# Kernel optimization log

Measured on AMD Instinct MI355X. Metric: run time of the kernel, lower is better.

The kernel has to match this reference:

```python
import jax, jax.numpy as jnp
import numpy as np

EPS = 1e-5
GROUPS = 8


def conv2d(x, w, b, pad):
    y = jax.lax.conv_general_dilated(
        x, w, window_strides=(1, 1), padding=[(pad, pad), (pad, pad)],
        dimension_numbers=('NCHW', 'OIHW', 'NCHW'))
    return y + b[None, :, None, None]


def setup_inputs() -> dict:
    key = jax.random.key(0)
    ks = jax.random.split(key, 8)
    b, c, h, w = 32, 256, 56, 56
    cg = c // GROUPS
    x = jax.random.normal(ks[0], (b, c, h, w), dtype=jnp.float32)
    w1 = jax.random.normal(ks[1], (cg, cg, 1, 1), dtype=jnp.float32) * 0.05
    b1 = jnp.zeros((cg,), dtype=jnp.float32)
    w3a = jax.random.normal(ks[2], (cg, cg, 3, 3), dtype=jnp.float32) * 0.05
    b3a = jnp.zeros((cg,), dtype=jnp.float32)
    w3b = jax.random.normal(ks[3], (c, c, 3, 3), dtype=jnp.float32) * 0.02
    b3b = jnp.zeros((c,), dtype=jnp.float32)
    gn_w = jnp.ones((cg,), dtype=jnp.float32)
    gn_b = jnp.zeros((cg,), dtype=jnp.float32)
    return {"x": x, "w1": w1, "b1": b1, "w3a": w3a, "b3a": b3a,
            "w3b": w3b, "b3b": b3b, "gn_w": gn_w, "gn_b": gn_b}


def reference(x, w1, b1, w3a, b3a, w3b, b3b, gn_w, gn_b):
    b, c, h, w = x.shape
    cg = c // GROUPS
    bg = b * GROUPS
    gx = x.reshape(bg, cg, h, w)

    # spatial attention on grouped channels
    x_h = gx.mean(axis=3, keepdims=True)                       # [bg,cg,h,1]
    x_w = gx.mean(axis=2, keepdims=True).transpose(0, 1, 3, 2)  # [bg,cg,w,1]
    hw = conv2d(jnp.concatenate([x_h, x_w], axis=2), w1, b1, 0)
    xh, xw = hw[:, :, :h], hw[:, :, h:]
    x0 = gx * jax.nn.sigmoid(xh) * jax.nn.sigmoid(xw.transpose(0, 1, 3, 2))

    # GroupNorm with num_groups == num_channels (per-channel over HxW)
    mu = x0.mean(axis=(2, 3), keepdims=True)
    var = x0.var(axis=(2, 3), keepdims=True)
    x1 = (x0 - mu) / jnp.sqrt(var + EPS) * gn_w[None, :, None, None] + gn_b[None, :, None, None]

    x2 = conv2d(gx, w3a, b3a, 1)

    # channel softmax-matmul attention (per group)
    x11 = jax.nn.softmax(x1.mean(axis=(2, 3)), axis=-1)[:, None, :]  # [bg,1,cg]
    x12 = x1.reshape(bg, cg, h * w)
    x21 = jax.nn.softmax(x2.mean(axis=(2, 3)), axis=-1)[:, None, :]
    x22 = x2.reshape(bg, cg, h * w)
    weights1 = (jnp.matmul(x11, x22) + jnp.matmul(x21, x12)).reshape(bg, 1, h, w)

    # BatchNorm2d(affine=False), batch statistics (training mode)
    xr = x0.reshape(b, c, h, w)
    bm = xr.mean(axis=(0, 2, 3), keepdims=True)
    bv = xr.var(axis=(0, 2, 3), keepdims=True)
    x3 = (xr - bm) / jnp.sqrt(bv + EPS)

    x4 = conv2d(x, w3b, b3b, 1)

    # spatial softmax-matmul attention over full channels
    x31 = jax.nn.softmax(x3.mean(axis=1).reshape(b, 1, h * w), axis=-1)  # [b,1,hw]
    x32 = x3.reshape(b, c, h * w).transpose(0, 2, 1)                     # [b,hw,c]
    x41 = jax.nn.softmax(x4.mean(axis=1).reshape(b, 1, h * w), axis=-1)
    x42 = x4.reshape(b, c, h * w).transpose(0, 2, 1)
    weights2 = (jnp.matmul(x31, x42) + jnp.matmul(x41, x32)).reshape(b, c, 1, 1)

    return (gx * jax.nn.sigmoid(weights1)).reshape(b, c, h, w) + x * jax.nn.sigmoid(weights2)
```

## Files before the change

### kernel.cpp

```cpp
#include <hip/hip_runtime.h>
#include <math.h>

#define B  32
#define C  256
#define HH 56
#define WW 56
#define HW 3136
#define G  8
#define CG 32
#define BG 256
#define GC 8192
#define EPSF 1e-5f

typedef __attribute__((ext_vector_type(8))) short short8;
typedef __attribute__((ext_vector_type(4))) float f32x4;

#define GLOAD16(g, l) __builtin_amdgcn_global_load_lds( \
    (const __attribute__((address_space(1))) void*)(g), \
    (__attribute__((address_space(3))) void*)(l), 16, 0, 0)

__device__ __forceinline__ float sigmoidf_(float v){ return 1.0f/(1.0f+__expf(-v)); }
__device__ __forceinline__ unsigned short f2bf(float v){
  unsigned u = __builtin_bit_cast(unsigned, v);
  u = u + 0x7FFFu + ((u>>16)&1u);
  return (unsigned short)(u>>16);
}

__global__ void k1_rowcol(const float* __restrict__ x, float* __restrict__ rowm, float* __restrict__ colm){
  int gc = blockIdx.x;
  __shared__ float t[56][57];
  const float* xp = x + (size_t)gc*HW;
  for(int idx=threadIdx.x; idx<HW; idx+=blockDim.x) t[idx/56][idx%56] = xp[idx];
  __syncthreads();
  int tid = threadIdx.x;
  if(tid < 56){
    float s=0.f;
    #pragma unroll 8
    for(int j=0;j<56;j++) s+=t[tid][j];
    rowm[gc*56+tid] = s*(1.0f/56.0f);
  } else if(tid>=64 && tid<120){
    int j=tid-64; float s=0.f;
    #pragma unroll 8
    for(int i=0;i<56;i++) s+=t[i][j];
    colm[gc*56+j] = s*(1.0f/56.0f);
  }
}

__global__ void k2_hw(const float* __restrict__ rowm, const float* __restrict__ colm,
                      const float* __restrict__ w1, const float* __restrict__ b1,
                      float* __restrict__ sh, float* __restrict__ sw){
  int bg = blockIdx.x;
  __shared__ float inb[32][112];
  __shared__ float wt[32*32];
  __shared__ float bb[32];
  for(int idx=threadIdx.x; idx<32*56; idx+=blockDim.x){
    int ic=idx/56, p=idx%56;
    inb[ic][p]    = rowm[(bg*32+ic)*56+p];
    inb[ic][56+p] = colm[(bg*32+ic)*56+p];
  }
  for(int idx=threadIdx.x; idx<1024; idx+=blockDim.x) wt[idx]=w1[idx];
  if(threadIdx.x<32) bb[threadIdx.x]=b1[threadIdx.x];
  __syncthreads();
  for(int o=threadIdx.x; o<32*112; o+=blockDim.x){
    int oc=o/112, p=o%112;
    float s=bb[oc];
    #pragma unroll
    for(int ic=0;ic<32;ic++) s += wt[oc*32+ic]*inb[ic][p];
    float sg = sigmoidf_(s);
    if(p<56) sh[(bg*32+oc)*56+p]=sg; else sw[(bg*32+oc)*56+(p-56)]=sg;
  }
}

__global__ void k2b_x11(const float* __restrict__ gnb, const float* __restrict__ b3a, float* __restrict__ x11){
  __shared__ float v[32];
  if(threadIdx.x<32) v[threadIdx.x]=gnb[threadIdx.x];
  __syncthreads();
  if(threadIdx.x==0){
    float m=-1e30f; for(int i=0;i<32;i++) m=fmaxf(m,v[i]);
    float s=0.f; for(int i=0;i<32;i++){ v[i]=__expf(v[i]-m); s+=v[i]; }
    float d=0.f;
    for(int i=0;i<32;i++){ float p=v[i]/s; x11[i]=p; d+=p*b3a[i]; }
    x11[32]=d;
  }
}

__global__ void k3_stats(const float* __restrict__ x, const float* __restrict__ sh, const float* __restrict__ sw,
                         float* __restrict__ gsum, float* __restrict__ gsq){
  int gc=blockIdx.x;
  __shared__ float ssh[56], ssw[56];
  if(threadIdx.x<56) ssh[threadIdx.x]=sh[gc*56+threadIdx.x];
  else if(threadIdx.x>=64&&threadIdx.x<120) ssw[threadIdx.x-64]=sw[gc*56+threadIdx.x-64];
  __syncthreads();
  const float* xp=x+(size_t)gc*HW;
  float s=0.f,s2=0.f;
  for(int p=threadIdx.x;p<HW;p+=blockDim.x){
    float v=xp[p]*ssh[p/56]*ssw[p%56];
    s+=v; s2+=v*v;
  }
  for(int off=32;off>0;off>>=1){ s+=__shfl_down(s,off,64); s2+=__shfl_down(s2,off,64); }
  __shared__ float rs[4], rs2[4];
  int wid=threadIdx.x>>6, lane=threadIdx.x&63;
  if(lane==0){rs[wid]=s; rs2[wid]=s2;}
  __syncthreads();
  if(threadIdx.x==0){
    gsum[gc]=rs[0]+rs[1]+rs[2]+rs[3];
    gsq[gc]=rs2[0]+rs2[1]+rs2[2]+rs2[3];
  }
}

__global__ void k4a(const float* __restrict__ gsum, const float* __restrict__ gsq,
                    float* __restrict__ mu, float* __restrict__ istd){
  int gc=blockIdx.x*256+threadIdx.x;
  float m=gsum[gc]*(1.0f/HW);
  float v=gsq[gc]*(1.0f/HW)-m*m;
  mu[gc]=m; istd[gc]=rsqrtf(v+EPSF);
}

__global__ void k4b(const float* __restrict__ gsum, const float* __restrict__ gsq,
                    float* __restrict__ bm, float* __restrict__ binv){
  int c=threadIdx.x;
  float s=0.f,s2=0.f;
  for(int b=0;b<B;b++){ s+=gsum[b*256+c]; s2+=gsq[b*256+c]; }
  float m=s*(1.0f/(B*HW));
  float v=s2*(1.0f/(B*HW))-m*m;
  bm[c]=m; binv[c]=rsqrtf(v+EPSF);
}

__global__ __launch_bounds__(128) void k5m(const unsigned short* __restrict__ xt,
    const unsigned short* __restrict__ wta, const float* __restrict__ x11,
    float* __restrict__ w1a, float* __restrict__ cs2){
  __shared__ short Bs[6*58*32];
  int bid = blockIdx.x;
  int xcd = bid & 7; int idx = bid >> 3;
  int b = xcd + 8*(idx/112); int idx2 = idx % 112;
  int g = idx2 / 14; int pt = idx2 % 14;
  int bg = b*8 + g;
  int i0 = pt*4;
  int tid = threadIdx.x;
  int lane = tid & 63, wv = tid >> 6;
  int q = lane >> 4, rl = lane & 15;
  const unsigned short* xb = xt + (size_t)b*58*58*256 + g*32;

  #pragma unroll
  for(int issue=0; issue<11; ++issue){
    int idxl = issue*128 + tid;
    if(idxl < 1392){
      int pl = idxl >> 2, ch = idxl & 3;
      int r = pl / 58, jj = pl - r*58;
      const unsigned short* src = xb + ((size_t)(i0 + r)*58 + jj)*256 + ((ch ^ ((pl>>1)&3))<<3);
      GLOAD16(src, &Bs[idxl*8]);
    }
  }
  __syncthreads();

  f32x4 acc[2][7];
  #pragma unroll
  for(int mi=0;mi<2;mi++)
    #pragma unroll
    for(int ni=0;ni<7;ni++) acc[mi][ni]=(f32x4){0.f,0.f,0.f,0.f};

  int pr[7], pj[7];
  #pragma unroll
  for(int ni=0;ni<7;ni++){
    int px = wv*112 + ni*16 + rl;
    pr[ni] = px/56; pj[ni] = px - pr[ni]*56;
  }

  for(int tap=0; tap<9; ++tap){
    int dy = tap/3, dx = tap - dy*3;
    short8 a[2], bfr[7];
    #pragma unroll
    for(int mi=0;mi<2;mi++)
      a[mi] = *(const short8*)(wta + tap*1024 + (mi*16+rl)*32 + q*8);
    #pragma unroll
    for(int ni=0;ni<7;ni++){
      int pix = (pr[ni] + dy)*58 + pj[ni] + dx;
      int cs = q ^ ((pix>>1)&3);
      bfr[ni] = *(const short8*)&Bs[pix*32 + cs*8];
    }
    #pragma unroll
    for(int mi=0;mi<2;mi++)
      #pragma unroll
      for(int ni=0;ni<7;ni++)
        acc[mi][ni] = __builtin_amdgcn_mfma_f32_16x16x32_bf16(a[mi], bfr[ni], acc[mi][ni], 0,0,0);
  }

  float x11v[2][4];
  #pragma unroll
  for(int mi=0;mi<2;mi++)
    #pragma unroll
    for(int r=0;r<4;r++) x11v[mi][r] = x11[mi*16 + q*4 + r];
  float x11b = x11[32];
  size_t pxg0 = (size_t)bg*HW + i0*56 + wv*112;
  #pragma unroll
  for(int ni=0;ni<7;ni++){
    float s=0.f;
    #pragma unroll
    for(int mi=0;mi<2;mi++)
      #pragma unroll
      for(int r=0;r<4;r++) s += x11v[mi][r]*acc[mi][ni][r];
    s += __shfl_xor(s,16,64);
    s += __shfl_xor(s,32,64);
    if(lane<16) w1a[pxg0 + ni*16 + lane] = s + x11b;
  }
  #pragma unroll
  for(int mi=0;mi<2;mi++){
    #pragma unroll
    for(int r=0;r<4;r++){
      float s=0.f;
      #pragma unroll
      for(int ni=0;ni<7;ni++) s += acc[mi][ni][r];
      s += __shfl_xor(s,1,64);
      s += __shfl_xor(s,2,64);
      s += __shfl_xor(s,4,64);
      s += __shfl_xor(s,8,64);
      if(rl==0) atomicAdd(&cs2[bg*32 + mi*16 + q*4 + r], s);
    }
  }
}

__global__ void k6(const float* __restrict__ cs2, const float* __restrict__ b3a,
                   const float* __restrict__ mu, const float* __restrict__ istd,
                   const float* __restrict__ gnw, const float* __restrict__ gnb,
                   float* __restrict__ av, float* __restrict__ cst){
  int bg=blockIdx.x; int t=threadIdx.x;
  float m = cs2[bg*32+t]*(1.0f/HW) + b3a[t];
  float mx=m;
  for(int off=16;off>0;off>>=1) mx=fmaxf(mx,__shfl_xor(mx,off,32));
  float e=__expf(m-mx);
  float s=e;
  for(int off=16;off>0;off>>=1) s+=__shfl_xor(s,off,32);
  float x21=e/s;
  int gc=bg*32+t;
  float is=istd[gc];
  av[gc]=x21*is*gnw[t];
  float cv=x21*(gnb[t]-mu[gc]*is*gnw[t]);
  for(int off=16;off>0;off>>=1) cv+=__shfl_xor(cv,off,32);
  if(t==0) cst[bg]=cv;
}

__global__ void k7(const float* __restrict__ x, const float* __restrict__ sh, const float* __restrict__ sw,
                   const float* __restrict__ w1a, const float* __restrict__ av, const float* __restrict__ cst,
                   const float* __restrict__ binv, float* __restrict__ sg1, float* __restrict__ s3pre){
  int b=blockIdx.x/56, i=blockIdx.x%56;
  int j=threadIdx.x;
  if(j>=56) return;
  float s3=0.f;
  for(int g=0;g<8;g++){
    int bg=b*8+g;
    float wsum=0.f;
    for(int cgi=0;cgi<32;cgi++){
      int gc=bg*32+cgi;
      int c=g*32+cgi;
      float x0=x[(size_t)gc*HW+i*56+j]*sh[gc*56+i]*sw[gc*56+j];
      wsum+=av[gc]*x0;
      s3+=binv[c]*x0;
    }
    sg1[(size_t)bg*HW+i*56+j]=sigmoidf_(w1a[(size_t)bg*HW+i*56+j]+wsum+cst[bg]);
  }
  s3pre[(size_t)b*HW+i*56+j]=s3*(1.0f/256.0f);
}

__global__ void k_softmax_hw(const float* __restrict__ in, float* __restrict__ out, float scale){
  int b=blockIdx.x;
  const float* ip=in+(size_t)b*HW;
  float mx=-1e30f;
  for(int p=threadIdx.x;p<HW;p+=blockDim.x) mx=fmaxf(mx,ip[p]*scale);
  for(int off=32;off>0;off>>=1) mx=fmaxf(mx,__shfl_xor(mx,off,64));
  __shared__ float red[4];
  int wid=threadIdx.x>>6, lane=threadIdx.x&63;
  if(lane==0) red[wid]=mx;
  __syncthreads();
  mx=fmaxf(fmaxf(red[0],red[1]),fmaxf(red[2],red[3]));
  float s=0.f;
  for(int p=threadIdx.x;p<HW;p+=blockDim.x) s+=__expf(ip[p]*scale-mx);
  for(int off=32;off>0;off>>=1) s+=__shfl_down(s,off,64);
  __shared__ float red2[4];
  if(lane==0) red2[wid]=s;
  __syncthreads();
  s=red2[0]+red2[1]+red2[2]+red2[3];
  float inv=1.0f/s;
  for(int p=threadIdx.x;p<HW;p+=blockDim.x) out[(size_t)b*HW+p]=__expf(ip[p]*scale-mx)*inv;
}

__global__ void kxt(const float* __restrict__ x, unsigned short* __restrict__ xt){
  int bid = blockIdx.x;
  int b = bid / 196; int r2 = bid % 196; int icb = r2 / 49; int pxb = r2 % 49;
  __shared__ float t[64][65];
  int tid = threadIdx.x;
  #pragma unroll
  for(int k=0;k<16;k++){
    int e = k*256 + tid;
    int ic = e>>6, px = e&63;
    t[ic][px] = x[((size_t)(b*256 + icb*64 + ic))*HW + pxb*64 + px];
  }
  __syncthreads();
  #pragma unroll
  for(int k=0;k<16;k++){
    int e = k*256 + tid;
    int px = e>>6, ic = e&63;
    int pxg = pxb*64 + px;
    int pi = pxg/56, pj = pxg%56;
    xt[(((size_t)b*58 + pi + 1)*58 + pj + 1)*256 + icb*64 + ic] = f2bf(t[ic][px]);
  }
}

__global__ void khalo(unsigned short* __restrict__ xt){
  int bid = blockIdx.x;
  int b = bid/228, hp = bid%228;
  int pi, pj;
  if(hp<58){pi=0;pj=hp;}
  else if(hp<116){pi=57;pj=hp-58;}
  else if(hp<172){pi=hp-116+1;pj=0;}
  else {pi=hp-172+1;pj=57;}
  xt[(((size_t)b*58+pi)*58+pj)*256 + threadIdx.x] = 0;
}

__global__ void kwt(const float* __restrict__ w3b, unsigned short* __restrict__ wt){
  int idx = blockIdx.x*256 + threadIdx.x;
  int tap = idx >> 16; int r = idx & 65535; int oc = r >> 8; int ic = r & 255;
  wt[idx] = f2bf(w3b[((size_t)oc*256 + ic)*9 + tap]);
}

__global__ void kwta(const float* __restrict__ w3a, unsigned short* __restrict__ wta){
  int idx = blockIdx.x*256 + threadIdx.x;
  if(idx < 9216){
    int tap = idx >> 10; int r = idx & 1023; int oc = r >> 5; int ic = r & 31;
    wta[idx] = f2bf(w3a[((size_t)oc*32 + ic)*9 + tap]);
  }
}

__global__ __launch_bounds__(512) void k9m(const unsigned short* __restrict__ xt,
    const unsigned short* __restrict__ wt, const float* __restrict__ x31,
    float* __restrict__ s4pre, float* __restrict__ w2a){
  __shared__ short Ab[2][128*32];
  __shared__ short Bb[2][224*32];
  int bid = blockIdx.x;
  int xcd = bid & 7; int idx = bid >> 3;
  int b = xcd + 8*(idx/28); int rr = idx % 28;
  int pt = rr >> 1; int oct = rr & 1;
  int i0 = pt*4; int ocb = oct*128;
  int tid = threadIdx.x;
  int lane = tid & 63, wv = tid >> 6;
  int wm = wv & 3, wn = wv >> 2;
  int q = lane >> 4, rl = lane & 15;
  const unsigned short* xb = xt + (size_t)b*58*58*256;

  #define STAGE_A(BUF, TAP, IC0) do{ \
    int idxl = tid; int oc_ = idxl>>2, cs_ = idxl&3; \
    const unsigned short* src = wt + (((size_t)(TAP)*256 + ocb + oc_)*256 + (IC0) + (((cs_ ^ ((oc_>>1)&3)))<<3)); \
    GLOAD16(src, &Ab[BUF][idxl*8]); }while(0)
  #define STAGE_B(BUF, TAP, IC0) do{ \
    int dy_ = (TAP)/3, dx_ = (TAP)%3; \
    { int idxl = tid; int px_ = idxl>>2, cs_ = idxl&3; int r_ = px_/56, j_ = px_ - r_*56; \
      const unsigned short* src = xb + ((size_t)((i0 + r_ + dy_)*58 + (j_ + dx_)))*256 + (IC0) + ((cs_ ^ ((px_>>1)&3))<<3); \
      GLOAD16(src, &Bb[BUF][idxl*8]); } \
    if(tid < 384){ int idxl = tid + 512; int px_ = idxl>>2, cs_ = idxl&3; int r_ = px_/56, j_ = px_ - r_*56; \
      const unsigned short* src = xb + ((size_t)((i0 + r_ + dy_)*58 + (j_ + dx_)))*256 + (IC0) + ((cs_ ^ ((px_>>1)&3))<<3); \
      GLOAD16(src, &Bb[BUF][idxl*8]); } }while(0)

  STAGE_A(0, 0, 0);
  STAGE_B(0, 0, 0);
  __syncthreads();

  f32x4 acc[2][7];
  #pragma unroll
  for(int mi=0;mi<2;mi++)
    #pragma unroll
    for(int ni=0;ni<7;ni++) acc[mi][ni] = (f32x4){0.f,0.f,0.f,0.f};

  for(int t=0; t<72; ++t){
    int cur = t & 1;
    if(t+1 < 72){
      int tn = t+1; int tap = tn >> 3; int ic0 = (tn & 7) << 5;
      STAGE_A(cur^1, tap, ic0);
      STAGE_B(cur^1, tap, ic0);
    }
    short8 a[2], bf[7];
    #pragma unroll
    for(int mi=0;mi<2;mi++){
      int row = wm*32 + mi*16 + rl;
      int cs = q ^ ((row>>1)&3);
      a[mi] = *(const short8*)&Ab[cur][row*32 + cs*8];
    }
    #pragma unroll
    for(int ni=0;ni<7;ni++){
      int px = wn*112 + ni*16 + rl;
      int cs = q ^ ((px>>1)&3);
      bf[ni] = *(const short8*)&Bb[cur][px*32 + cs*8];
    }
    #pragma unroll
    for(int mi=0;mi<2;mi++)
      #pragma unroll
      for(int ni=0;ni<7;ni++)
        acc[mi][ni] = __builtin_amdgcn_mfma_f32_16x16x32_bf16(a[mi], bf[ni], acc[mi][ni], 0,0,0);
    __syncthreads();
  }
  #undef STAGE_A
  #undef STAGE_B

  size_t pxbase = (size_t)b*HW + i0*56 + wn*112;
  #pragma unroll
  for(int ni=0;ni<7;ni++){
    float s = 0.f;
    #pragma unroll
    for(int mi=0;mi<2;mi++){
      s += acc[mi][ni][0]+acc[mi][ni][1]+acc[mi][ni][2]+acc[mi][ni][3];
    }
    s += __shfl_xor(s, 16, 64);
    s += __shfl_xor(s, 32, 64);
    if(lane < 16) atomicAdd(&s4pre[pxbase + ni*16 + lane], s);
  }
  float x31v[7];
  #pragma unroll
  for(int ni=0;ni<7;ni++) x31v[ni] = x31[pxbase + ni*16 + rl];
  #pragma unroll
  for(int mi=0;mi<2;mi++){
    #pragma unroll
    for(int r=0;r<4;r++){
      float s = 0.f;
      #pragma unroll
      for(int ni=0;ni<7;ni++) s += x31v[ni]*acc[mi][ni][r];
      s += __shfl_xor(s, 1, 64);
      s += __shfl_xor(s, 2, 64);
      s += __shfl_xor(s, 4, 64);
      s += __shfl_xor(s, 8, 64);
      if(rl == 0) atomicAdd(&w2a[b*256 + ocb + wm*32 + mi*16 + q*4 + r], s);
    }
  }
}

__global__ __launch_bounds__(256) void k11f(const float* __restrict__ x, const float* __restrict__ sh,
    const float* __restrict__ sw, const float* __restrict__ x41, const float* __restrict__ bm,
    const float* __restrict__ binv, const float* __restrict__ w2a, const float* __restrict__ b3b,
    const float* __restrict__ sg1, float* __restrict__ out){
  int gc=blockIdx.x; int b=gc>>8, c=gc&255, bg=gc>>5;
  __shared__ float xs[HW];
  __shared__ float ssh[56], ssw[56];
  __shared__ float red[4];
  int tid=threadIdx.x;
  if(tid<56) ssh[tid]=sh[gc*56+tid];
  else if(tid>=64&&tid<120) ssw[tid-64]=sw[gc*56+tid-64];
  const float* xp=x+(size_t)gc*HW;
  const float* wp=x41+(size_t)b*HW;
  for(int p=tid;p<HW;p+=256) xs[p]=xp[p];
  __syncthreads();
  float s=0.f;
  for(int p=tid;p<HW;p+=256){
    float x0=xs[p]*ssh[p/56]*ssw[p%56];
    s+=wp[p]*x0;
  }
  for(int off=32;off>0;off>>=1) s+=__shfl_down(s,off,64);
  int wid=tid>>6, lane=tid&63;
  if(lane==0) red[wid]=s;
  __syncthreads();
  float t=red[0]+red[1]+red[2]+red[3];
  float sg2=sigmoidf_(w2a[gc]+b3b[c]+binv[c]*t-bm[c]*binv[c]);
  const float* sp=sg1+(size_t)bg*HW;
  float* op=out+(size_t)gc*HW;
  for(int p=tid;p<HW;p+=256){
    op[p]=xs[p]*(sp[p]+sg2);
  }
}

extern "C" void kernel_launch(void* const* d_in, const int* in_sizes, int n_in,
                              void* d_out, int out_size, void* d_ws, size_t ws_size,
                              hipStream_t stream) {
  const float* x   = (const float*)d_in[0];
  const float* w1  = (const float*)d_in[1];
  const float* b1  = (const float*)d_in[2];
  const float* w3a = (const float*)d_in[3];
  const float* b3a = (const float*)d_in[4];
  const float* w3b = (const float*)d_in[5];
  const float* b3b = (const float*)d_in[6];
  const float* gnw = (const float*)d_in[7];
  const float* gnb = (const float*)d_in[8];
  float* out=(float*)d_out;
  float* ws=(float*)d_ws;

  float* rowm=ws;
  float* colm=rowm+458752;
  float* sh  =colm+458752;
  float* sw  =sh+458752;
  float* x11 =sw+458752;
  float* gsum=x11+64;
  float* gsq =gsum+8192;
  float* mu  =gsq+8192;
  float* istd=mu+8192;
  float* bm  =istd+8192;
  float* binv=bm+256;
  float* cs2 =binv+256;
  float* w1a =cs2+8192;
  float* av  =w1a+802816;
  float* cst =av+8192;
  float* s3  =cst+256;
  float* x31 =s3+100352;
  float* s4  =x31+100352;
  float* x41 =s4+100352;
  float* w2a =x41+100352;
  float* w2  =w2a+8192;
  float* sg1 =w2+8192;
  unsigned short* xt = (unsigned short*)(sg1 + 802816);
  unsigned short* wtb = xt + (size_t)32*58*58*256;
  unsigned short* wta = wtb + 589824;

  kxt<<<32*4*49,256,0,stream>>>(x, xt);
  khalo<<<32*228,256,0,stream>>>(xt);
  kwt<<<2304,256,0,stream>>>(w3b, wtb);
  kwta<<<36,256,0,stream>>>(w3a, wta);

  k1_rowcol<<<GC,256,0,stream>>>(x,rowm,colm);
  k2_hw<<<BG,128,0,stream>>>(rowm,colm,w1,b1,sh,sw);
  k2b_x11<<<1,32,0,stream>>>(gnb,b3a,x11);
  k3_stats<<<GC,256,0,stream>>>(x,sh,sw,gsum,gsq);
  k4a<<<32,256,0,stream>>>(gsum,gsq,mu,istd);
  k4b<<<1,256,0,stream>>>(gsum,gsq,bm,binv);
  hipMemsetAsync(cs2,0,8192*sizeof(float),stream);
  k5m<<<256*14,128,0,stream>>>(xt,wta,x11,w1a,cs2);
  k6<<<BG,32,0,stream>>>(cs2,b3a,mu,istd,gnw,gnb,av,cst);
  k7<<<B*56,64,0,stream>>>(x,sh,sw,w1a,av,cst,binv,sg1,s3);
  k_softmax_hw<<<B,256,0,stream>>>(s3,x31,1.0f);
  hipMemsetAsync(w2a,0,8192*sizeof(float),stream);
  hipMemsetAsync(s4,0,(size_t)HW*B*sizeof(float),stream);
  k9m<<<32*28,512,0,stream>>>(xt,wtb,x31,s4,w2a);
  k_softmax_hw<<<B,256,0,stream>>>(s4,x41,1.0f/256.0f);
  k11f<<<GC,256,0,stream>>>(x,sh,sw,x41,bm,binv,w2a,b3b,sg1,out);
}
```

Before: 391.1 us.

## Fuse bf16 transpose with row/column means and read bf16 NHWC in k7

Merges the bf16 NHWC transpose kernel with the row/column mean kernel so x is read once for both, with column sums accumulated atomically into a zeroed buffer and scaled later in k2. k2 also writes channel-last copies of the sigmoid gates so the rewritten k7 can read the bf16 transposed input with coalesced 16-byte loads and shuffle reductions, in place of the strided fp32 reads of x. The softmax kernels are launched with 512 threads. In exchange, k7 now uses bf16-rounded x (a precision loss), k2 writes extra buffers, and the fused kernel runs only 512 blocks.

```diff
diff --git a/kernel.cpp b/kernel.cpp
--- a/kernel.cpp
+++ b/kernel.cpp
@@ -25,38 +25,76 @@
   u = u + 0x7FFFu + ((u>>16)&1u);
   return (unsigned short)(u>>16);
 }
-
-__global__ void k1_rowcol(const float* __restrict__ x, float* __restrict__ rowm, float* __restrict__ colm){
-  int gc = blockIdx.x;
-  __shared__ float t[56][57];
-  const float* xp = x + (size_t)gc*HW;
-  for(int idx=threadIdx.x; idx<HW; idx+=blockDim.x) t[idx/56][idx%56] = xp[idx];
-  __syncthreads();
+__device__ __forceinline__ float bf2f(unsigned short v){
+  return __builtin_bit_cast(float, ((unsigned)v)<<16);
+}
+
+__global__ __launch_bounds__(256) void k1x(const float* __restrict__ x, unsigned short* __restrict__ xt,
+    float* __restrict__ rowm, float* __restrict__ colm){
+  int bid = blockIdx.x;
+  int b = bid>>4; int icb = (bid>>1)&7; int rh = bid&1;
+  __shared__ float tile[32][57];
+  __shared__ float colacc[32][56];
   int tid = threadIdx.x;
-  if(tid < 56){
-    float s=0.f;
-    #pragma unroll 8
-    for(int j=0;j<56;j++) s+=t[tid][j];
-    rowm[gc*56+tid] = s*(1.0f/56.0f);
-  } else if(tid>=64 && tid<120){
-    int j=tid-64; float s=0.f;
-    #pragma unroll 8
-    for(int i=0;i<56;i++) s+=t[i][j];
-    colm[gc*56+j] = s*(1.0f/56.0f);
-  }
+  for(int e=tid; e<1792; e+=256) colacc[e/56][e%56] = 0.f;
+  __syncthreads();
+  const float* xb = x + ((size_t)b*256 + icb*32)*HW;
+  for(int ii=0; ii<28; ++ii){
+    int i = rh*28 + ii;
+    for(int e=tid; e<1792; e+=256){
+      int ch=e/56, j=e%56;
+      tile[ch][j] = xb[(size_t)ch*HW + i*56 + j];
+    }
+    __syncthreads();
+    if(tid<32){
+      float s=0.f;
+      #pragma unroll 8
+      for(int j=0;j<56;j++) s += tile[tid][j];
+      rowm[((size_t)b*256 + icb*32 + tid)*56 + i] = s*(1.0f/56.0f);
+    }
+    for(int e=tid; e<1792; e+=256){
+      int ch=e/56, j=e%56;
+      colacc[ch][j] += tile[ch][j];
+    }
+    if(tid<224){
+      int j = tid>>2, k = tid&3;
+      short8 v;
+      #pragma unroll
+      for(int m=0;m<8;m++) v[m] = (short)f2bf(tile[k*8+m][j]);
+      *(short8*)(xt + (((size_t)b*58 + i+1)*58 + (j+1))*256 + icb*32 + k*8) = v;
+    }
+    __syncthreads();
+  }
+  for(int e=tid; e<1792; e+=256){
+    int ch=e/56, j=e%56;
+    atomicAdd(&colm[((size_t)b*256+icb*32+ch)*56 + j], colacc[ch][j]);
+  }
+}
+
+__global__ void khalo(unsigned short* __restrict__ xt){
+  int bid = blockIdx.x;
+  int b = bid/228, hp = bid%228;
+  int pi, pj;
+  if(hp<58){pi=0;pj=hp;}
+  else if(hp<116){pi=57;pj=hp-58;}
+  else if(hp<172){pi=hp-116+1;pj=0;}
+  else {pi=hp-172+1;pj=57;}
+  xt[(((size_t)b*58+pi)*58+pj)*256 + threadIdx.x] = 0;
 }
 
 __global__ void k2_hw(const float* __restrict__ rowm, const float* __restrict__ colm,
                       const float* __restrict__ w1, const float* __restrict__ b1,
-                      float* __restrict__ sh, float* __restrict__ sw){
+                      float* __restrict__ sh, float* __restrict__ sw,
+                      float* __restrict__ shT, float* __restrict__ swT){
   int bg = blockIdx.x;
+  int b = bg>>3, g = bg&7;
   __shared__ float inb[32][112];
   __shared__ float wt[32*32];
   __shared__ float bb[32];
   for(int idx=threadIdx.x; idx<32*56; idx+=blockDim.x){
     int ic=idx/56, p=idx%56;
     inb[ic][p]    = rowm[(bg*32+ic)*56+p];
-    inb[ic][56+p] = colm[(bg*32+ic)*56+p];
+    inb[ic][56+p] = colm[(bg*32+ic)*56+p]*(1.0f/56.0f);
   }
   for(int idx=threadIdx.x; idx<1024; idx+=blockDim.x) wt[idx]=w1[idx];
   if(threadIdx.x<32) bb[threadIdx.x]=b1[threadIdx.x];
@@ -67,7 +105,14 @@
     #pragma unroll
     for(int ic=0;ic<32;ic++) s += wt[oc*32+ic]*inb[ic][p];
     float sg = sigmoidf_(s);
-    if(p<56) sh[(bg*32+oc)*56+p]=sg; else sw[(bg*32+oc)*56+(p-56)]=sg;
+    int c = g*32+oc;
+    if(p<56){
+      sh[(bg*32+oc)*56+p]=sg;
+      shT[((size_t)b*56+p)*256 + c]=sg;
+    } else {
+      sw[(bg*32+oc)*56+(p-56)]=sg;
+      swT[((size_t)b*56+(p-56))*256 + c]=sg;
+    }
   }
 }
 
@@ -239,26 +284,50 @@
   if(t==0) cst[bg]=cv;
 }
 
-__global__ void k7(const float* __restrict__ x, const float* __restrict__ sh, const float* __restrict__ sw,
-                   const float* __restrict__ w1a, const float* __restrict__ av, const float* __restrict__ cst,
-                   const float* __restrict__ binv, float* __restrict__ sg1, float* __restrict__ s3pre){
-  int b=blockIdx.x/56, i=blockIdx.x%56;
-  int j=threadIdx.x;
-  if(j>=56) return;
-  float s3=0.f;
-  for(int g=0;g<8;g++){
-    int bg=b*8+g;
-    float wsum=0.f;
-    for(int cgi=0;cgi<32;cgi++){
-      int gc=bg*32+cgi;
-      int c=g*32+cgi;
-      float x0=x[(size_t)gc*HW+i*56+j]*sh[gc*56+i]*sw[gc*56+j];
-      wsum+=av[gc]*x0;
-      s3+=binv[c]*x0;
-    }
-    sg1[(size_t)bg*HW+i*56+j]=sigmoidf_(w1a[(size_t)bg*HW+i*56+j]+wsum+cst[bg]);
-  }
-  s3pre[(size_t)b*HW+i*56+j]=s3*(1.0f/256.0f);
+__global__ __launch_bounds__(256) void k7x(const unsigned short* __restrict__ xt,
+    const float* __restrict__ shT, const float* __restrict__ swT,
+    const float* __restrict__ av, const float* __restrict__ binv, const float* __restrict__ cst,
+    const float* __restrict__ w1a, float* __restrict__ sg1, float* __restrict__ s3pre){
+  int bid = blockIdx.x; int b = bid/56, i = bid%56;
+  __shared__ float shs[256], avs[256], bins[256], cst8[8];
+  int tid = threadIdx.x;
+  shs[tid]  = shT[((size_t)b*56+i)*256 + tid];
+  avs[tid]  = av[b*256 + tid];
+  bins[tid] = binv[tid];
+  if(tid<8) cst8[tid] = cst[b*8+tid];
+  __syncthreads();
+  int h = tid>>5, l = tid&31;
+  int bg = l>>2;
+  int c0 = l*8;
+  float sh8[8], av8[8], bi8[8];
+  #pragma unroll
+  for(int m=0;m<8;m++){ sh8[m]=shs[c0+m]; av8[m]=avs[c0+m]; bi8[m]=bins[c0+m]; }
+  float cstv = cst8[bg];
+  for(int pass=0; pass<7; ++pass){
+    int j = pass*8 + h;
+    short8 xv = *(const short8*)(xt + (((size_t)b*58 + i+1)*58 + j+1)*256 + c0);
+    const float* swp = swT + ((size_t)b*56 + j)*256 + c0;
+    float ws=0.f, s3=0.f;
+    #pragma unroll
+    for(int m=0;m<8;m++){
+      float x0 = bf2f((unsigned short)xv[m]) * sh8[m] * swp[m];
+      ws += av8[m]*x0;
+      s3 += bi8[m]*x0;
+    }
+    ws += __shfl_xor(ws,1,64);
+    ws += __shfl_xor(ws,2,64);
+    s3 += __shfl_xor(s3,1,64);
+    s3 += __shfl_xor(s3,2,64);
+    s3 += __shfl_xor(s3,4,64);
+    s3 += __shfl_xor(s3,8,64);
+    s3 += __shfl_xor(s3,16,64);
+    int p = i*56 + j;
+    if((l&3)==0){
+      size_t o = ((size_t)(b*8+bg))*HW + p;
+      sg1[o] = sigmoidf_(w1a[o] + ws + cstv);
+    }
+    if(l==0) s3pre[(size_t)b*HW + p] = s3*(1.0f/256.0f);
+  }
 }
 
 __global__ void k_softmax_hw(const float* __restrict__ in, float* __restrict__ out, float scale){
@@ -267,53 +336,24 @@
   float mx=-1e30f;
   for(int p=threadIdx.x;p<HW;p+=blockDim.x) mx=fmaxf(mx,ip[p]*scale);
   for(int off=32;off>0;off>>=1) mx=fmaxf(mx,__shfl_xor(mx,off,64));
-  __shared__ float red[4];
+  __shared__ float red[8];
   int wid=threadIdx.x>>6, lane=threadIdx.x&63;
   if(lane==0) red[wid]=mx;
   __syncthreads();
-  mx=fmaxf(fmaxf(red[0],red[1]),fmaxf(red[2],red[3]));
+  mx=red[0];
+  #pragma unroll
+  for(int w=1;w<8;w++) mx=fmaxf(mx,red[w]);
   float s=0.f;
   for(int p=threadIdx.x;p<HW;p+=blockDim.x) s+=__expf(ip[p]*scale-mx);
   for(int off=32;off>0;off>>=1) s+=__shfl_down(s,off,64);
-  __shared__ float red2[4];
+  __shared__ float red2[8];
   if(lane==0) red2[wid]=s;
   __syncthreads();
-  s=red2[0]+red2[1]+red2[2]+red2[3];
+  s=red2[0];
+  #pragma unroll
+  for(int w=1;w<8;w++) s+=red2[w];
   float inv=1.0f/s;
   for(int p=threadIdx.x;p<HW;p+=blockDim.x) out[(size_t)b*HW+p]=__expf(ip[p]*scale-mx)*inv;
-}
-
-__global__ void kxt(const float* __restrict__ x, unsigned short* __restrict__ xt){
-  int bid = blockIdx.x;
-  int b = bid / 196; int r2 = bid % 196; int icb = r2 / 49; int pxb = r2 % 49;
-  __shared__ float t[64][65];
-  int tid = threadIdx.x;
-  #pragma unroll
-  for(int k=0;k<16;k++){
-    int e = k*256 + tid;
-    int ic = e>>6, px = e&63;
-    t[ic][px] = x[((size_t)(b*256 + icb*64 + ic))*HW + pxb*64 + px];
-  }
-  __syncthreads();
-  #pragma unroll
-  for(int k=0;k<16;k++){
-    int e = k*256 + tid;
-    int px = e>>6, ic = e&63;
-    int pxg = pxb*64 + px;
-    int pi = pxg/56, pj = pxg%56;
-    xt[(((size_t)b*58 + pi + 1)*58 + pj + 1)*256 + icb*64 + ic] = f2bf(t[ic][px]);
-  }
-}
-
-__global__ void khalo(unsigned short* __restrict__ xt){
-  int bid = blockIdx.x;
-  int b = bid/228, hp = bid%228;
-  int pi, pj;
-  if(hp<58){pi=0;pj=hp;}
-  else if(hp<116){pi=57;pj=hp-58;}
-  else if(hp<172){pi=hp-116+1;pj=0;}
-  else {pi=hp-172+1;pj=57;}
-  xt[(((size_t)b*58+pi)*58+pj)*256 + threadIdx.x] = 0;
 }
 
 __global__ void kwt(const float* __restrict__ w3b, unsigned short* __restrict__ wt){
@@ -498,19 +538,20 @@
   float* s4  =x31+100352;
   float* x41 =s4+100352;
   float* w2a =x41+100352;
-  float* w2  =w2a+8192;
-  float* sg1 =w2+8192;
+  float* shT =w2a+8192;
+  float* swT =shT+458752;
+  float* sg1 =swT+458752;
   unsigned short* xt = (unsigned short*)(sg1 + 802816);
   unsigned short* wtb = xt + (size_t)32*58*58*256;
   unsigned short* wta = wtb + 589824;
 
-  kxt<<<32*4*49,256,0,stream>>>(x, xt);
+  hipMemsetAsync(colm, 0, 458752*sizeof(float), stream);
+  k1x<<<512,256,0,stream>>>(x, xt, rowm, colm);
   khalo<<<32*228,256,0,stream>>>(xt);
   kwt<<<2304,256,0,stream>>>(w3b, wtb);
   kwta<<<36,256,0,stream>>>(w3a, wta);
 
-  k1_rowcol<<<GC,256,0,stream>>>(x,rowm,colm);
-  k2_hw<<<BG,128,0,stream>>>(rowm,colm,w1,b1,sh,sw);
+  k2_hw<<<BG,128,0,stream>>>(rowm,colm,w1,b1,sh,sw,shT,swT);
   k2b_x11<<<1,32,0,stream>>>(gnb,b3a,x11);
   k3_stats<<<GC,256,0,stream>>>(x,sh,sw,gsum,gsq);
   k4a<<<32,256,0,stream>>>(gsum,gsq,mu,istd);
@@ -518,11 +559,11 @@
   hipMemsetAsync(cs2,0,8192*sizeof(float),stream);
   k5m<<<256*14,128,0,stream>>>(xt,wta,x11,w1a,cs2);
   k6<<<BG,32,0,stream>>>(cs2,b3a,mu,istd,gnw,gnb,av,cst);
-  k7<<<B*56,64,0,stream>>>(x,sh,sw,w1a,av,cst,binv,sg1,s3);
-  k_softmax_hw<<<B,256,0,stream>>>(s3,x31,1.0f);
+  k7x<<<B*56,256,0,stream>>>(xt,shT,swT,av,binv,cst,w1a,sg1,s3);
+  k_softmax_hw<<<B,512,0,stream>>>(s3,x31,1.0f);
   hipMemsetAsync(w2a,0,8192*sizeof(float),stream);
   hipMemsetAsync(s4,0,(size_t)HW*B*sizeof(float),stream);
   k9m<<<32*28,512,0,stream>>>(xt,wtb,x31,s4,w2a);
-  k_softmax_hw<<<B,256,0,stream>>>(s4,x41,1.0f/256.0f);
+  k_softmax_hw<<<B,512,0,stream>>>(s4,x41,1.0f/256.0f);
   k11f<<<GC,256,0,stream>>>(x,sh,sw,x41,bm,binv,w2a,b3b,sg1,out);
 }
```

Result: slower. 415.5 us (+6.2%).
